# Performance work log

Hardware: AMD Instinct MI355X
Metric: run time of the kernel (lower is better)

Reference implementation:

```python
import jax, jax.numpy as jnp
import numpy as np

B, L, H = 16, 4096, 256

def setup_inputs() -> dict:
    key = jax.random.key(0)
    k1, k2, k3 = jax.random.split(key, 3)
    scale = 1.0 / np.sqrt(H)
    x = jax.random.normal(k1, (B, L, H), dtype=jnp.float32)
    Wv = jax.random.normal(k2, (H, H), dtype=jnp.float32) * scale  # value_proj weight (torch Linear: y = x @ W.T)
    Wo = jax.random.normal(k3, (H, H), dtype=jnp.float32) * scale  # out_proj weight
    return {"x": x, "Wv": Wv, "Wo": Wo}

def reference(x, Wv, Wo):
    # x: [B, L, H]
    Bx, Lx, Hx = x.shape
    # Causal uniform-average 'attention' matrix: T[i, j] = 1/(i+1) for j <= i, else 0.
    tril = jnp.tril(jnp.ones((Lx, Lx), dtype=x.dtype))
    counts = jnp.arange(1, Lx + 1, dtype=x.dtype)[:, None]  # row-wise counts = i+1
    T = tril / counts
    # v = out_proj(value_proj(x)); torch Linear applies W.T on the right
    v = (x @ Wv.T) @ Wo.T                       # [B, L, H]
    # mixed[b, i] = mean over j <= i of v[b, j]  (== causal cumulative mean)
    mixed = jnp.einsum('ij,bjh->bih', T, v)     # [B, L, H]
    # dropout is identity in eval mode; pre_ln residual
    return x + mixed
```

## Files before the change

### kernel.cpp

```cpp
#include <hip/hip_runtime.h>
#include <hip/hip_bf16.h>


#define B_  16
#define L_  4096
#define H_  256
#define M_  (B_*L_)
#define CH  64
#define CHROWS 64
#define BM 128

typedef short short4v __attribute__((ext_vector_type(4)));
typedef short short8  __attribute__((ext_vector_type(8)));
typedef float f32x4   __attribute__((ext_vector_type(4)));

__device__ __forceinline__ unsigned short f2bf(float f) {
  unsigned int u = __builtin_bit_cast(unsigned int, f);
  u += 0x7fffu + ((u >> 16) & 1u);
  return (unsigned short)(u >> 16);
}
__device__ __forceinline__ float bf2f(unsigned short s) {
  unsigned int u = ((unsigned int)s) << 16;
  return __builtin_bit_cast(float, u);
}

__global__ void fuse_w_kernel(const float* __restrict__ Wv,
                              const float* __restrict__ Wo,
                              unsigned short* __restrict__ Wbf) {
  __shared__ float wo[H_];
  int h = blockIdx.x, t = threadIdx.x;
  wo[t] = Wo[h*H_ + t];
  __syncthreads();
  float acc = 0.f;
  #pragma unroll 8
  for (int m = 0; m < H_; ++m) acc += wo[m] * Wv[m*H_ + t];
  Wbf[h*H_ + t] = f2bf(acc);
}

__global__ void partial_kernel(const float* __restrict__ x, float* __restrict__ P) {
  int c = blockIdx.x, b = blockIdx.y, t = threadIdx.x;
  const float* p = x + ((size_t)(b*L_ + c*CHROWS))*H_ + t;
  float s = 0.f;
  #pragma unroll 8
  for (int r = 0; r < CHROWS; ++r) s += p[(size_t)r*H_];
  P[(b*CH + c)*H_ + t] = s;
}

__global__ void scan_kernel(const float* __restrict__ P, float* __restrict__ O) {
  int b = blockIdx.x, t = threadIdx.x;
  float run = 0.f;
  #pragma unroll
  for (int c = 0; c < CH; ++c) {
    int idx = (b*CH + c)*H_ + t;
    O[idx] = run;
    run += P[idx];
  }
}

__global__ __launch_bounds__(512, 4) void main_kernel(
    const float* __restrict__ x,
    const unsigned short* __restrict__ Wbf,
    const float* __restrict__ Op,
    float* __restrict__ out) {
  extern __shared__ char smem[];
  float* zbuf = (float*)(smem + 65536);
  float* csum = zbuf + 256;

  const int tid = threadIdx.x;
  const int lane = tid & 63, wave = tid >> 6;
  const int rowBase = blockIdx.x * BM;

  #pragma unroll 4
  for (int it = 0; it < 16; ++it) {
    int r = it*8 + wave;
    const float4 v = *(const float4*)(x + (size_t)(rowBase + r)*H_ + lane*4);
    short4v s;
    s[0] = (short)f2bf(v.x); s[1] = (short)f2bf(v.y);
    s[2] = (short)f2bf(v.z); s[3] = (short)f2bf(v.w);
    *(short4v*)(smem + r*512 + ((lane*8) ^ ((r & 7) << 4))) = s;
  }
  __syncthreads();

  if (tid < H_) {
    const float* op = Op + (size_t)blockIdx.x * 2 * H_;
    float z = 0.f;
    #pragma unroll 4
    for (int kk = 0; kk < 32; ++kk) {
      short8 w8 = *(const short8*)(Wbf + (size_t)tid*H_ + kk*8);
      #pragma unroll
      for (int e = 0; e < 8; ++e)
        z += op[kk*8 + e] * bf2f((unsigned short)w8[e]);
    }
    zbuf[tid] = z;
  }

  const int wr = wave >> 2, wc = wave & 3;
  const int lrow = lane & 15, g = lane >> 4;

  f32x4 acc[4][4] = {};
  #pragma unroll
  for (int k0 = 0; k0 < H_; k0 += 64) {
    #pragma unroll
    for (int ks = 0; ks < 2; ++ks) {
      short8 bfr[4], af[4];
      #pragma unroll
      for (int n = 0; n < 4; ++n) {
        int wrow = wc*64 + n*16 + lrow;
        bfr[n] = *(const short8*)(Wbf + (size_t)wrow*H_ + k0 + ks*32 + g*8);
      }
      #pragma unroll
      for (int i = 0; i < 4; ++i) {
        int ar = wr*64 + i*16 + lrow;
        int cb = (k0*2 + ks*64 + g*16) ^ ((ar & 7) << 4);
        af[i] = *(const short8*)(smem + ar*512 + cb);
      }
      #pragma unroll
      for (int i = 0; i < 4; ++i)
        #pragma unroll
        for (int n = 0; n < 4; ++n)
          acc[i][n] = __builtin_amdgcn_mfma_f32_16x16x32_bf16(af[i], bfr[n], acc[i][n], 0, 0, 0);
    }
  }

  #pragma unroll
  for (int n = 0; n < 4; ++n) {
    float run = 0.f;
    #pragma unroll
    for (int i = 0; i < 4; ++i) {
      f32x4 a = acc[i][n];
      a[1] += a[0]; a[2] += a[1]; a[3] += a[2];
      float Bv = a[3];
      float v = Bv;
      float t = __shfl_up(v, 16);
      if (lane >= 16) v += t;
      t = __shfl_up(v, 32);
      if (lane >= 32) v += t;
      float gex = v - Bv;
      float tot = __shfl(v, lrow + 48);
      float addv = gex + run;
      a[0] += addv; a[1] += addv; a[2] += addv; a[3] += addv;
      acc[i][n] = a;
      run += tot;
    }
    if (wr == 0 && g == 0) csum[wc*64 + n*16 + lrow] = run;
  }
  __syncthreads();

  float base[4];
  #pragma unroll
  for (int n = 0; n < 4; ++n) {
    int c = wc*64 + n*16 + lrow;
    base[n] = zbuf[c] + (wr ? csum[c] : 0.f);
  }
  #pragma unroll
  for (int i = 0; i < 4; ++i) {
    #pragma unroll
    for (int q = 0; q < 4; ++q) {
      int row = rowBase + wr*64 + i*16 + g*4 + q;
      float scale = 1.0f / (float)((row & (L_-1)) + 1);
      size_t rb = (size_t)row * H_;
      #pragma unroll
      for (int n = 0; n < 4; ++n) {
        int c = wc*64 + n*16 + lrow;
        out[rb + c] = x[rb + c] + (acc[i][n][q] + base[n]) * scale;
      }
    }
  }
}

extern "C" void kernel_launch(void* const* d_in, const int* in_sizes, int n_in,
                              void* d_out, int out_size, void* d_ws, size_t ws_size,
                              hipStream_t stream) {
  const float* x  = (const float*)d_in[0];
  const float* Wv = (const float*)d_in[1];
  const float* Wo = (const float*)d_in[2];
  float* out = (float*)d_out;

  char* ws = (char*)d_ws;
  unsigned short* Wbf = (unsigned short*)ws;
  float* P  = (float*)(ws + 131072);
  float* Op = (float*)(ws + 131072 + 1048576);

  hipLaunchKernelGGL(fuse_w_kernel,  dim3(H_),     dim3(H_), 0, stream, Wv, Wo, Wbf);
  hipLaunchKernelGGL(partial_kernel, dim3(CH, B_), dim3(H_), 0, stream, x, P);
  hipLaunchKernelGGL(scan_kernel,    dim3(B_),     dim3(H_), 0, stream, P, Op);
  hipLaunchKernelGGL(main_kernel,    dim3(M_/BM),  dim3(512), 67584, stream,
                     x, Wbf, Op, out);
}
```

Measured before the change: 84.92 us.

## Halve main tile rows, keep x in registers, stage output through LDS for coalesced stores

The main kernel tile shrinks from 128 to 64 rows, and all 8 waves now split the columns instead of 2x4 rows by columns. This removes the cross-wave column-sum exchange and one barrier. The x rows are loaded once into registers and reused for the residual add, so x is no longer reread from global memory with scattered per-element accesses. The scaled results go through LDS so the output is written as coalesced float4 rows. The z prefix dot product is split across all 512 threads. The cost is twice as many blocks, each recomputing the z vector, plus extra LDS traffic and more register pressure.

```diff
diff --git a/kernel.cpp b/kernel.cpp
--- a/kernel.cpp
+++ b/kernel.cpp
@@ -8,7 +8,7 @@
 #define M_  (B_*L_)
 #define CH  64
 #define CHROWS 64
-#define BM 128
+#define BM 64
 
 typedef short short4v __attribute__((ext_vector_type(4)));
 typedef short short8  __attribute__((ext_vector_type(8)));
@@ -20,8 +20,7 @@
   return (unsigned short)(u >> 16);
 }
 __device__ __forceinline__ float bf2f(unsigned short s) {
-  unsigned int u = ((unsigned int)s) << 16;
-  return __builtin_bit_cast(float, u);
+  return __builtin_bit_cast(float, ((unsigned int)s) << 16);
 }
 
 __global__ void fuse_w_kernel(const float* __restrict__ Wv,
@@ -62,109 +61,122 @@
     const unsigned short* __restrict__ Wbf,
     const float* __restrict__ Op,
     float* __restrict__ out) {
-  extern __shared__ char smem[];
-  float* zbuf = (float*)(smem + 65536);
-  float* csum = zbuf + 256;
+  __shared__ __align__(16) char smem[69632];
+  float* zpart = (float*)(smem + 67584);
 
   const int tid = threadIdx.x;
   const int lane = tid & 63, wave = tid >> 6;
   const int rowBase = blockIdx.x * BM;
 
-  #pragma unroll 4
-  for (int it = 0; it < 16; ++it) {
-    int r = it*8 + wave;
-    const float4 v = *(const float4*)(x + (size_t)(rowBase + r)*H_ + lane*4);
-    short4v s;
-    s[0] = (short)f2bf(v.x); s[1] = (short)f2bf(v.y);
-    s[2] = (short)f2bf(v.z); s[3] = (short)f2bf(v.w);
-    *(short4v*)(smem + r*512 + ((lane*8) ^ ((r & 7) << 4))) = s;
-  }
-  __syncthreads();
-
-  if (tid < H_) {
-    const float* op = Op + (size_t)blockIdx.x * 2 * H_;
+  float4 xk[8];
+  const float* xb = x + (size_t)rowBase * H_;
+  #pragma unroll
+  for (int j = 0; j < 8; ++j)
+    xk[j] = *(const float4*)(xb + (j*8 + wave)*H_ + lane*4);
+
+  {
+    const int c = tid & 255, h = tid >> 8;
+    const float* op = Op + (size_t)blockIdx.x * H_ + h*128;
+    const unsigned short* wr = Wbf + (size_t)c * H_ + h*128;
     float z = 0.f;
     #pragma unroll 4
-    for (int kk = 0; kk < 32; ++kk) {
-      short8 w8 = *(const short8*)(Wbf + (size_t)tid*H_ + kk*8);
-      #pragma unroll
-      for (int e = 0; e < 8; ++e)
-        z += op[kk*8 + e] * bf2f((unsigned short)w8[e]);
+    for (int kk = 0; kk < 16; ++kk) {
+      short8 w8 = *(const short8*)(wr + kk*8);
+      #pragma unroll
+      for (int e = 0; e < 8; ++e) z += op[kk*8 + e] * bf2f((unsigned short)w8[e]);
     }
-    zbuf[tid] = z;
-  }
-
-  const int wr = wave >> 2, wc = wave & 3;
+    zpart[h*256 + c] = z;
+  }
+
+  #pragma unroll
+  for (int j = 0; j < 8; ++j) {
+    int r = j*8 + wave;
+    short4v s;
+    s[0] = (short)f2bf(xk[j].x); s[1] = (short)f2bf(xk[j].y);
+    s[2] = (short)f2bf(xk[j].z); s[3] = (short)f2bf(xk[j].w);
+    *(short4v*)(smem + r*512 + ((lane*8) ^ ((r & 7) << 4))) = s;
+  }
+  __syncthreads();
+
+  const int wc = wave;
   const int lrow = lane & 15, g = lane >> 4;
-
-  f32x4 acc[4][4] = {};
-  #pragma unroll
-  for (int k0 = 0; k0 < H_; k0 += 64) {
+  f32x4 acc[4][2] = {};
+  #pragma unroll
+  for (int k0 = 0; k0 < 4; ++k0) {
     #pragma unroll
     for (int ks = 0; ks < 2; ++ks) {
-      short8 bfr[4], af[4];
-      #pragma unroll
-      for (int n = 0; n < 4; ++n) {
-        int wrow = wc*64 + n*16 + lrow;
-        bfr[n] = *(const short8*)(Wbf + (size_t)wrow*H_ + k0 + ks*32 + g*8);
+      short8 bfr[2], af[4];
+      #pragma unroll
+      for (int n = 0; n < 2; ++n) {
+        int wrow = wc*32 + n*16 + lrow;
+        bfr[n] = *(const short8*)(Wbf + (size_t)wrow*H_ + k0*64 + ks*32 + g*8);
       }
       #pragma unroll
       for (int i = 0; i < 4; ++i) {
-        int ar = wr*64 + i*16 + lrow;
-        int cb = (k0*2 + ks*64 + g*16) ^ ((ar & 7) << 4);
+        int ar = i*16 + lrow;
+        int cb = (k0*128 + ks*64 + g*16) ^ ((ar & 7) << 4);
         af[i] = *(const short8*)(smem + ar*512 + cb);
       }
       #pragma unroll
       for (int i = 0; i < 4; ++i)
         #pragma unroll
-        for (int n = 0; n < 4; ++n)
+        for (int n = 0; n < 2; ++n)
           acc[i][n] = __builtin_amdgcn_mfma_f32_16x16x32_bf16(af[i], bfr[n], acc[i][n], 0, 0, 0);
     }
   }
 
-  #pragma unroll
-  for (int n = 0; n < 4; ++n) {
+  float base[2];
+  #pragma unroll
+  for (int n = 0; n < 2; ++n) {
+    int c = wc*32 + n*16 + lrow;
+    base[n] = zpart[c] + zpart[256 + c];
+  }
+  #pragma unroll
+  for (int n = 0; n < 2; ++n) {
     float run = 0.f;
     #pragma unroll
     for (int i = 0; i < 4; ++i) {
       f32x4 a = acc[i][n];
       a[1] += a[0]; a[2] += a[1]; a[3] += a[2];
       float Bv = a[3];
-      float v = Bv;
-      float t = __shfl_up(v, 16);
-      if (lane >= 16) v += t;
-      t = __shfl_up(v, 32);
-      if (lane >= 32) v += t;
+      float v = Bv, t;
+      t = __shfl_up(v, 16); if (lane >= 16) v += t;
+      t = __shfl_up(v, 32); if (lane >= 32) v += t;
       float gex = v - Bv;
       float tot = __shfl(v, lrow + 48);
-      float addv = gex + run;
-      a[0] += addv; a[1] += addv; a[2] += addv; a[3] += addv;
+      float addv = gex + run + base[n];
+      #pragma unroll
+      for (int q = 0; q < 4; ++q) {
+        int row = rowBase + i*16 + g*4 + q;
+        float scale = 1.0f / (float)((row & (L_-1)) + 1);
+        a[q] = (a[q] + addv) * scale;
+      }
       acc[i][n] = a;
       run += tot;
     }
-    if (wr == 0 && g == 0) csum[wc*64 + n*16 + lrow] = run;
-  }
-  __syncthreads();
-
-  float base[4];
-  #pragma unroll
-  for (int n = 0; n < 4; ++n) {
-    int c = wc*64 + n*16 + lrow;
-    base[n] = zbuf[c] + (wr ? csum[c] : 0.f);
-  }
-  #pragma unroll
-  for (int i = 0; i < 4; ++i) {
+  }
+  __syncthreads();
+
+  #pragma unroll
+  for (int i = 0; i < 4; ++i)
     #pragma unroll
-    for (int q = 0; q < 4; ++q) {
-      int row = rowBase + wr*64 + i*16 + g*4 + q;
-      float scale = 1.0f / (float)((row & (L_-1)) + 1);
-      size_t rb = (size_t)row * H_;
-      #pragma unroll
-      for (int n = 0; n < 4; ++n) {
-        int c = wc*64 + n*16 + lrow;
-        out[rb + c] = x[rb + c] + (acc[i][n][q] + base[n]) * scale;
-      }
-    }
+    for (int n = 0; n < 2; ++n)
+      #pragma unroll
+      for (int q = 0; q < 4; ++q) {
+        int row = i*16 + g*4 + q, col = wc*32 + n*16 + lrow;
+        *(float*)(smem + row*1040 + col*4) = acc[i][n][q];
+      }
+  __syncthreads();
+
+  float* ob = out + (size_t)rowBase * H_;
+  #pragma unroll
+  for (int j = 0; j < 8; ++j) {
+    int r = j*8 + wave;
+    f32x4 y = *(const f32x4*)(smem + r*1040 + lane*16);
+    float4 o;
+    o.x = xk[j].x + y[0]; o.y = xk[j].y + y[1];
+    o.z = xk[j].z + y[2]; o.w = xk[j].w + y[3];
+    *(float4*)(ob + r*H_ + lane*4) = o;
   }
 }
 
@@ -184,6 +196,6 @@
   hipLaunchKernelGGL(fuse_w_kernel,  dim3(H_),     dim3(H_), 0, stream, Wv, Wo, Wbf);
   hipLaunchKernelGGL(partial_kernel, dim3(CH, B_), dim3(H_), 0, stream, x, P);
   hipLaunchKernelGGL(scan_kernel,    dim3(B_),     dim3(H_), 0, stream, P, Op);
-  hipLaunchKernelGGL(main_kernel,    dim3(M_/BM),  dim3(512), 67584, stream,
+  hipLaunchKernelGGL(main_kernel,    dim3(M_/BM),  dim3(512), 0, stream,
                      x, Wbf, Op, out);
 }
```

Measured after the change: 81.35 us. 4.2% less time.
